# Kernel tuning notes

Hardware: AMD Instinct MI355X
Metric: run time of the kernel (lower is better)

The kernel has to match this reference:

```python
import jax, jax.numpy as jnp
import numpy as np

B, C, D, H, W, N = 1, 48, 64, 64, 64, 16


def setup_inputs() -> dict:
    key = jax.random.key(0)
    ks = jax.random.split(key, 7)
    x = jax.random.normal(ks[0], (B, C, D, H, W), jnp.float32)
    # Per-direction S6 parameters (3 scan directions: D, H, W axes)
    A_log = jax.random.normal(ks[1], (3, C, N), jnp.float32) * 0.5
    W_dt = jax.random.normal(ks[2], (3, C, C), jnp.float32) * (0.5 / np.sqrt(C))
    b_dt = jax.random.normal(ks[3], (3, C), jnp.float32) * 0.1
    W_B = jax.random.normal(ks[4], (3, C, N), jnp.float32) / np.sqrt(C)
    W_C = jax.random.normal(ks[5], (3, C, N), jnp.float32) / np.sqrt(C)
    D_skip = jnp.ones((3, C), jnp.float32)
    return dict(x=x, A_log=A_log, W_dt=W_dt, b_dt=b_dt, W_B=W_B, W_C=W_C, D_skip=D_skip)


def _dir_scan(xl, dt, Bc, Cc, A, Dskip, axis):
    """Selective scan along one spatial axis.
    xl, dt: [B,D,H,W,C]; Bc, Cc: [B,D,H,W,N]; A: [C,N]; Dskip: [C]."""
    L = xl.shape[axis]

    def to_seq(t):
        t = jnp.moveaxis(t, axis, 0)          # [L, ..., F]
        return t.reshape(L, -1, t.shape[-1])  # [L, M, F]

    xs, dts, Bs, Cs = to_seq(xl), to_seq(dt), to_seq(Bc), to_seq(Cc)
    M = xs.shape[1]

    def step(h, inp):
        x_t, dt_t, B_t, C_t = inp              # [M,C],[M,C],[M,N],[M,N]
        decay = jnp.exp(dt_t[:, :, None] * A)  # [M,C,N]
        h = decay * h + (dt_t * x_t)[:, :, None] * B_t[:, None, :]
        y = jnp.einsum('mcn,mn->mc', h, C_t) + Dskip * x_t
        return h, y

    h0 = jnp.zeros((M, xs.shape[2], A.shape[-1]), xl.dtype)
    _, ys = jax.lax.scan(step, h0, (xs, dts, Bs, Cs))  # ys: [L, M, C]
    seq_shape = jnp.moveaxis(xl, axis, 0).shape
    return jnp.moveaxis(ys.reshape(seq_shape), 0, axis)


def reference(x, A_log, W_dt, b_dt, W_B, W_C, D_skip):
    xl = jnp.moveaxis(x, 1, -1)  # [B,D,H,W,C]
    y = jnp.zeros_like(xl)
    for d, axis in enumerate((1, 2, 3)):  # scan along D, H, W
        A = -jnp.exp(A_log[d])                       # [C,N], negative -> stable
        dt = jax.nn.softplus(xl @ W_dt[d] + b_dt[d])  # [B,D,H,W,C]
        Bc = xl @ W_B[d]                              # [B,D,H,W,N]
        Cc = xl @ W_C[d]                              # [B,D,H,W,N]
        y = y + _dir_scan(xl, dt, Bc, Cc, A, D_skip[d], axis)
    return jnp.moveaxis(y, -1, 1)  # [B,C,D,H,W]
```

## Files before the change

kernel.cpp:

```cpp
#include <hip/hip_runtime.h>
#include <math.h>

#define CCH 48
#define NST 16
#define VOX (64*64*64)

__device__ __forceinline__ float softplus_f(float s) {
    return fmaxf(s, 0.f) + log1pf(__expf(-fabsf(s)));
}

template<int CTRL>
__device__ __forceinline__ float dpp_add(float x) {
    int v = __builtin_amdgcn_update_dpp(0, __float_as_int(x), CTRL, 0xF, 0xF, true);
    return x + __int_as_float(v);
}

__global__ __launch_bounds__(256) void k_transpose_in(const float* __restrict__ x,
                                                      float* __restrict__ xt) {
    __shared__ float tile[CCH * 65];
    int v0 = blockIdx.x * 64;
    int t = threadIdx.x;
#pragma unroll
    for (int i = 0; i < 12; ++i) {
        int idx = t + i * 256;
        int c = idx >> 6, v = idx & 63;
        tile[c * 65 + v] = x[c * VOX + v0 + v];
    }
    __syncthreads();
#pragma unroll
    for (int i = 0; i < 12; ++i) {
        int idx = t + i * 256;
        int v = idx / CCH, c = idx - v * CCH;
        xt[(v0 + v) * CCH + c] = tile[c * 65 + v];
    }
}

__global__ __launch_bounds__(256) void k_transpose_out(const float* __restrict__ yws,
                                                       float* __restrict__ out) {
    __shared__ float tile[CCH * 65];
    int v0 = blockIdx.x * 64;
    int t = threadIdx.x;
#pragma unroll
    for (int i = 0; i < 12; ++i) {
        int idx = t + i * 256;
        int v = idx / CCH, c = idx - v * CCH;
        tile[c * 65 + v] = yws[(v0 + v) * CCH + c];
    }
    __syncthreads();
#pragma unroll
    for (int i = 0; i < 12; ++i) {
        int idx = t + i * 256;
        int c = idx >> 6, v = idx & 63;
        out[c * VOX + v0 + v] = tile[c * 65 + v];
    }
}

#define OFF_XS    0
#define OFF_WDT   3072
#define OFF_WB    5568
#define OFF_WC    6400
#define OFF_DTS   7232
#define OFF_UX    10496
#define OFF_BC    13760
#define OFF_CC    14848
#define OFF_YS    3072
#define SMEM_FLOATS 15936

__global__ __launch_bounds__(768, 6) void k_scan(
    const float* __restrict__ xt, float* __restrict__ yws,
    const float* __restrict__ A_log, const float* __restrict__ W_dt,
    const float* __restrict__ b_dt, const float* __restrict__ W_B,
    const float* __restrict__ W_C, const float* __restrict__ D_skip,
    int dir, int stride_v, int accumulate)
{
    __shared__ __align__(16) float smem[SMEM_FLOATS];
    float* xs   = smem + OFF_XS;
    float* wdtT = smem + OFF_WDT;
    float* wBT  = smem + OFF_WB;
    float* wCT  = smem + OFF_WC;
    float* dtsT = smem + OFF_DTS;
    float* uxT  = smem + OFF_UX;
    float* BcsT = smem + OFF_BC;
    float* CcsT = smem + OFF_CC;
    float* ys   = smem + OFF_YS;

    int t = threadIdx.x;
    int lid = blockIdx.x;
    int a = lid >> 6, b = lid & 63;
    int vbase;
    if (dir == 0) vbase = lid;
    else if (dir == 1) vbase = a * 4096 + b;
    else vbase = a * 4096 + b * 64;

    const float* wdt_g = W_dt + dir * CCH * CCH;
    const float* wB_g  = W_B + dir * CCH * NST;
    const float* wC_g  = W_C + dir * CCH * NST;

    {
        int q = t % 12, l = t / 12;
        *(float4*)&xs[l * CCH + 4 * q] =
            *(const float4*)&xt[(vbase + l * stride_v) * CCH + 4 * q];
    }
    for (int idx = t; idx < CCH * CCH; idx += 768) {
        int k = idx / CCH, c2 = idx - k * CCH;
        wdtT[c2 * 52 + k] = wdt_g[idx];
    }
    {
        int k = t >> 4, n2 = t & 15;
        wBT[n2 * 52 + k] = wB_g[t];
        wCT[n2 * 52 + k] = wC_g[t];
    }
    __syncthreads();

    {
        int c  = t % CCH;
        int l0 = t / CCH;
        float bc = b_dt[dir * CCH + c];
        const float4* wr  = (const float4*)&wdtT[c * 52];
        const float4* xr0 = (const float4*)&xs[(4 * l0 + 0) * CCH];
        const float4* xr1 = (const float4*)&xs[(4 * l0 + 1) * CCH];
        const float4* xr2 = (const float4*)&xs[(4 * l0 + 2) * CCH];
        const float4* xr3 = (const float4*)&xs[(4 * l0 + 3) * CCH];
        float s0 = bc, s1 = bc, s2 = bc, s3 = bc;
#pragma unroll
        for (int q = 0; q < 12; ++q) {
            float4 wv = wr[q];
            float4 x0 = xr0[q], x1 = xr1[q], x2 = xr2[q], x3 = xr3[q];
            s0 = fmaf(x0.x, wv.x, s0); s0 = fmaf(x0.y, wv.y, s0);
            s0 = fmaf(x0.z, wv.z, s0); s0 = fmaf(x0.w, wv.w, s0);
            s1 = fmaf(x1.x, wv.x, s1); s1 = fmaf(x1.y, wv.y, s1);
            s1 = fmaf(x1.z, wv.z, s1); s1 = fmaf(x1.w, wv.w, s1);
            s2 = fmaf(x2.x, wv.x, s2); s2 = fmaf(x2.y, wv.y, s2);
            s2 = fmaf(x2.z, wv.z, s2); s2 = fmaf(x2.w, wv.w, s2);
            s3 = fmaf(x3.x, wv.x, s3); s3 = fmaf(x3.y, wv.y, s3);
            s3 = fmaf(x3.z, wv.z, s3); s3 = fmaf(x3.w, wv.w, s3);
        }
        float4 dtv, uxv;
        dtv.x = softplus_f(s0); uxv.x = dtv.x * xs[(4 * l0 + 0) * CCH + c];
        dtv.y = softplus_f(s1); uxv.y = dtv.y * xs[(4 * l0 + 1) * CCH + c];
        dtv.z = softplus_f(s2); uxv.z = dtv.z * xs[(4 * l0 + 2) * CCH + c];
        dtv.w = softplus_f(s3); uxv.w = dtv.w * xs[(4 * l0 + 3) * CCH + c];
        *(float4*)&dtsT[c * 68 + 4 * l0] = dtv;
        *(float4*)&uxT[c * 68 + 4 * l0]  = uxv;
    }
    {
        int n = t & 15;
        int lA = t >> 4;
#pragma unroll
        for (int rep = 0; rep < 2; ++rep) {
            int l = (rep == 0) ? lA : (48 + lA);
            if (rep == 0 || t < 256) {
                const float4* xr  = (const float4*)&xs[l * CCH];
                const float4* wbr = (const float4*)&wBT[n * 52];
                const float4* wcr = (const float4*)&wCT[n * 52];
                float sB = 0.f, sC = 0.f;
#pragma unroll
                for (int q = 0; q < 12; ++q) {
                    float4 xv = xr[q];
                    float4 wb = wbr[q];
                    float4 wc = wcr[q];
                    sB = fmaf(xv.x, wb.x, sB); sC = fmaf(xv.x, wc.x, sC);
                    sB = fmaf(xv.y, wb.y, sB); sC = fmaf(xv.y, wc.y, sC);
                    sB = fmaf(xv.z, wb.z, sB); sC = fmaf(xv.z, wc.z, sC);
                    sB = fmaf(xv.w, wb.w, sB); sC = fmaf(xv.w, wc.w, sC);
                }
                BcsT[n * 68 + l] = sB;
                CcsT[n * 68 + l] = sC;
            }
        }
    }
    __syncthreads();

    if (t < 384) {
        int cc = t >> 3, nh = t & 7;
        float a0 = -expf(A_log[dir * CCH * NST + cc * NST + nh]);
        float a1 = -expf(A_log[dir * CCH * NST + cc * NST + nh + 8]);
        const float4* dt4 = (const float4*)&dtsT[cc * 68];
        const float4* ux4 = (const float4*)&uxT[cc * 68];
        const float4* B4a = (const float4*)&BcsT[nh * 68];
        const float4* B4b = (const float4*)&BcsT[(nh + 8) * 68];
        const float4* C4a = (const float4*)&CcsT[nh * 68];
        const float4* C4b = (const float4*)&CcsT[(nh + 8) * 68];
        float h0 = 0.f, h1 = 0.f;

#define STEP(COMP, LIDX)                                                    \
        {                                                                   \
            float e0 = __expf(dtv.COMP * a0);                               \
            float e1 = __expf(dtv.COMP * a1);                               \
            h0 = fmaf(e0, h0, uxv.COMP * Bva.COMP);                         \
            h1 = fmaf(e1, h1, uxv.COMP * Bvb.COMP);                         \
            float p = fmaf(h1, Cvb.COMP, h0 * Cva.COMP);                    \
            p = dpp_add<0xB1>(p);                                           \
            p = dpp_add<0x4E>(p);                                           \
            p = dpp_add<0x141>(p);                                          \
            if (nh == 0) ys[(LIDX) * CCH + cc] = p;                         \
        }

#pragma unroll
        for (int l4 = 0; l4 < 16; ++l4) {
            float4 dtv = dt4[l4];
            float4 uxv = ux4[l4];
            float4 Bva = B4a[l4];
            float4 Bvb = B4b[l4];
            float4 Cva = C4a[l4];
            float4 Cvb = C4b[l4];
            STEP(x, l4 * 4 + 0)
            STEP(y, l4 * 4 + 1)
            STEP(z, l4 * 4 + 2)
            STEP(w, l4 * 4 + 3)
        }
#undef STEP
    }
    __syncthreads();

    {
        int q = t % 12, l = t / 12;
        float4 yv = *(const float4*)&ys[l * CCH + 4 * q];
        float4 xv = *(const float4*)&xs[l * CCH + 4 * q];
        float4 dv = *(const float4*)&D_skip[dir * CCH + 4 * q];
        yv.x = fmaf(dv.x, xv.x, yv.x);
        yv.y = fmaf(dv.y, xv.y, yv.y);
        yv.z = fmaf(dv.z, xv.z, yv.z);
        yv.w = fmaf(dv.w, xv.w, yv.w);
        float* gp = &yws[(vbase + l * stride_v) * CCH + 4 * q];
        if (accumulate) {
            float4 old = *(const float4*)gp;
            yv.x += old.x; yv.y += old.y; yv.z += old.z; yv.w += old.w;
        }
        *(float4*)gp = yv;
    }
}

extern "C" void kernel_launch(void* const* d_in, const int* in_sizes, int n_in,
                              void* d_out, int out_size, void* d_ws, size_t ws_size,
                              hipStream_t stream) {
    const float* x      = (const float*)d_in[0];
    const float* A_log  = (const float*)d_in[1];
    const float* W_dt   = (const float*)d_in[2];
    const float* b_dt   = (const float*)d_in[3];
    const float* W_B    = (const float*)d_in[4];
    const float* W_C    = (const float*)d_in[5];
    const float* D_skip = (const float*)d_in[6];
    float* out = (float*)d_out;

    float* xt  = (float*)d_ws;
    float* yws = xt + (size_t)VOX * CCH;

    k_transpose_in<<<VOX / 64, 256, 0, stream>>>(x, xt);
    k_scan<<<4096, 768, 0, stream>>>(xt, yws, A_log, W_dt, b_dt, W_B, W_C, D_skip, 0, 4096, 0);
    k_scan<<<4096, 768, 0, stream>>>(xt, yws, A_log, W_dt, b_dt, W_B, W_C, D_skip, 1, 64, 1);
    k_scan<<<4096, 768, 0, stream>>>(xt, yws, A_log, W_dt, b_dt, W_B, W_C, D_skip, 2, 1, 1);
    k_transpose_out<<<VOX / 64, 256, 0, stream>>>(yws, out);
}
```

Baseline: 390.2 us.

## Compute dt/B/C projections with bf16 MFMA instead of scalar FMA

Replaces the per-thread fp32 FMA projections of x onto W_dt, W_B and W_C with one fused 80x48 by 48x64 matrix product on bf16 MFMA (16x16x32) instructions, using bf16 copies of x and the weights staged in shared memory with K padded to 64. This is meant to cut the VALU and LDS-read cost of the projection phase before the scan. In exchange it adds conversion work, an extra sync and some extra shared memory, and bf16 rounding of the projection inputs lowers precision, which could hurt accuracy.

Measured after the change: 360.8 us. 7.5% less time.

```diff
diff --git a/kernel.cpp b/kernel.cpp
--- a/kernel.cpp
+++ b/kernel.cpp
@@ -5,8 +5,18 @@
 #define NST 16
 #define VOX (64*64*64)
 
+typedef __attribute__((ext_vector_type(8))) short bf16x8_t;
+typedef __attribute__((ext_vector_type(4))) float f32x4_t;
+typedef unsigned short ushort_t;
+
 __device__ __forceinline__ float softplus_f(float s) {
     return fmaxf(s, 0.f) + log1pf(__expf(-fabsf(s)));
+}
+
+__device__ __forceinline__ ushort_t f2bf(float f) {
+    unsigned u = __float_as_uint(f);
+    unsigned r = (u + 0x7FFF + ((u >> 16) & 1)) >> 16;
+    return (ushort_t)r;
 }
 
 template<int CTRL>
@@ -56,15 +66,14 @@
 }
 
 #define OFF_XS    0
-#define OFF_WDT   3072
-#define OFF_WB    5568
-#define OFF_WC    6400
-#define OFF_DTS   7232
-#define OFF_UX    10496
-#define OFF_BC    13760
-#define OFF_CC    14848
+#define OFF_XB    3072
+#define OFF_WB16  5376
+#define OFF_DTS   8256
+#define OFF_UX    11520
+#define OFF_BC    14784
+#define OFF_CC    15872
 #define OFF_YS    3072
-#define SMEM_FLOATS 15936
+#define SMEM_FLOATS 16960
 
 __global__ __launch_bounds__(768, 6) void k_scan(
     const float* __restrict__ xt, float* __restrict__ yws,
@@ -75,14 +84,13 @@
 {
     __shared__ __align__(16) float smem[SMEM_FLOATS];
     float* xs   = smem + OFF_XS;
-    float* wdtT = smem + OFF_WDT;
-    float* wBT  = smem + OFF_WB;
-    float* wCT  = smem + OFF_WC;
     float* dtsT = smem + OFF_DTS;
     float* uxT  = smem + OFF_UX;
     float* BcsT = smem + OFF_BC;
     float* CcsT = smem + OFF_CC;
     float* ys   = smem + OFF_YS;
+    ushort_t* xb = (ushort_t*)(smem + OFF_XB);
+    ushort_t* wb = (ushort_t*)(smem + OFF_WB16);
 
     int t = threadIdx.x;
     int lid = blockIdx.x;
@@ -98,76 +106,66 @@
 
     {
         int q = t % 12, l = t / 12;
-        *(float4*)&xs[l * CCH + 4 * q] =
-            *(const float4*)&xt[(vbase + l * stride_v) * CCH + 4 * q];
-    }
-    for (int idx = t; idx < CCH * CCH; idx += 768) {
-        int k = idx / CCH, c2 = idx - k * CCH;
-        wdtT[c2 * 52 + k] = wdt_g[idx];
-    }
-    {
-        int k = t >> 4, n2 = t & 15;
-        wBT[n2 * 52 + k] = wB_g[t];
-        wCT[n2 * 52 + k] = wC_g[t];
-    }
-    __syncthreads();
-
-    {
-        int c  = t % CCH;
-        int l0 = t / CCH;
-        float bc = b_dt[dir * CCH + c];
-        const float4* wr  = (const float4*)&wdtT[c * 52];
-        const float4* xr0 = (const float4*)&xs[(4 * l0 + 0) * CCH];
-        const float4* xr1 = (const float4*)&xs[(4 * l0 + 1) * CCH];
-        const float4* xr2 = (const float4*)&xs[(4 * l0 + 2) * CCH];
-        const float4* xr3 = (const float4*)&xs[(4 * l0 + 3) * CCH];
-        float s0 = bc, s1 = bc, s2 = bc, s3 = bc;
-#pragma unroll
-        for (int q = 0; q < 12; ++q) {
-            float4 wv = wr[q];
-            float4 x0 = xr0[q], x1 = xr1[q], x2 = xr2[q], x3 = xr3[q];
-            s0 = fmaf(x0.x, wv.x, s0); s0 = fmaf(x0.y, wv.y, s0);
-            s0 = fmaf(x0.z, wv.z, s0); s0 = fmaf(x0.w, wv.w, s0);
-            s1 = fmaf(x1.x, wv.x, s1); s1 = fmaf(x1.y, wv.y, s1);
-            s1 = fmaf(x1.z, wv.z, s1); s1 = fmaf(x1.w, wv.w, s1);
-            s2 = fmaf(x2.x, wv.x, s2); s2 = fmaf(x2.y, wv.y, s2);
-            s2 = fmaf(x2.z, wv.z, s2); s2 = fmaf(x2.w, wv.w, s2);
-            s3 = fmaf(x3.x, wv.x, s3); s3 = fmaf(x3.y, wv.y, s3);
-            s3 = fmaf(x3.z, wv.z, s3); s3 = fmaf(x3.w, wv.w, s3);
-        }
+        float4 v = *(const float4*)&xt[(vbase + l * stride_v) * CCH + 4 * q];
+        *(float4*)&xs[l * CCH + 4 * q] = v;
+        unsigned p0 = (unsigned)f2bf(v.x) | ((unsigned)f2bf(v.y) << 16);
+        unsigned p1 = (unsigned)f2bf(v.z) | ((unsigned)f2bf(v.w) << 16);
+        unsigned* d = (unsigned*)&xb[l * 72 + 4 * q];
+        d[0] = p0; d[1] = p1;
+    }
+    for (int idx = t; idx < 3840; idx += 768) {
+        float v; int row, k;
+        if (idx < 2304)      { k = idx / 48;       row = idx % 48;        v = wdt_g[idx]; }
+        else if (idx < 3072) { int j = idx - 2304; k = j >> 4; row = 48 + (j & 15); v = wB_g[j]; }
+        else                 { int j = idx - 3072; k = j >> 4; row = 64 + (j & 15); v = wC_g[j]; }
+        wb[row * 72 + k] = f2bf(v);
+    }
+    for (int i = t; i < 80 * 16; i += 768) wb[(i >> 4) * 72 + 48 + (i & 15)] = 0;
+    for (int i = t; i < 64 * 16; i += 768) xb[(i >> 4) * 72 + 48 + (i & 15)] = 0;
+    __syncthreads();
+
+    {
+        int w = t >> 6, lane = t & 63;
+        if (w < 10) {
+            int r16 = lane & 15, g = lane >> 4;
+#pragma unroll
+            for (int tt = 0; tt < 2; ++tt) {
+                int tile = w * 2 + tt;
+                int tm = tile >> 2, tn = tile & 3;
+                const ushort_t* ap = &wb[(tm * 16 + r16) * 72 + g * 8];
+                const ushort_t* bp = &xb[(tn * 16 + r16) * 72 + g * 8];
+                bf16x8_t A0 = *(const bf16x8_t*)ap;
+                bf16x8_t A1 = *(const bf16x8_t*)(ap + 32);
+                bf16x8_t B0 = *(const bf16x8_t*)bp;
+                bf16x8_t B1 = *(const bf16x8_t*)(bp + 32);
+                f32x4_t acc = {0.f, 0.f, 0.f, 0.f};
+                acc = __builtin_amdgcn_mfma_f32_16x16x32_bf16(A0, B0, acc, 0, 0, 0);
+                acc = __builtin_amdgcn_mfma_f32_16x16x32_bf16(A1, B1, acc, 0, 0, 0);
+                int col = tn * 16 + r16;
+                float* outp;
+                if (tm < 3)       outp = &dtsT[(tm * 16 + g * 4) * 68 + col];
+                else if (tm == 3) outp = &BcsT[(g * 4) * 68 + col];
+                else              outp = &CcsT[(g * 4) * 68 + col];
+                outp[0 * 68] = acc[0];
+                outp[1 * 68] = acc[1];
+                outp[2 * 68] = acc[2];
+                outp[3 * 68] = acc[3];
+            }
+        }
+    }
+    __syncthreads();
+
+    {
+        int c = t % CCH, l0 = t / CCH;
+        float bias = b_dt[dir * CCH + c];
+        float4 dv = *(const float4*)&dtsT[c * 68 + 4 * l0];
         float4 dtv, uxv;
-        dtv.x = softplus_f(s0); uxv.x = dtv.x * xs[(4 * l0 + 0) * CCH + c];
-        dtv.y = softplus_f(s1); uxv.y = dtv.y * xs[(4 * l0 + 1) * CCH + c];
-        dtv.z = softplus_f(s2); uxv.z = dtv.z * xs[(4 * l0 + 2) * CCH + c];
-        dtv.w = softplus_f(s3); uxv.w = dtv.w * xs[(4 * l0 + 3) * CCH + c];
+        dtv.x = softplus_f(dv.x + bias); uxv.x = dtv.x * xs[(4 * l0 + 0) * CCH + c];
+        dtv.y = softplus_f(dv.y + bias); uxv.y = dtv.y * xs[(4 * l0 + 1) * CCH + c];
+        dtv.z = softplus_f(dv.z + bias); uxv.z = dtv.z * xs[(4 * l0 + 2) * CCH + c];
+        dtv.w = softplus_f(dv.w + bias); uxv.w = dtv.w * xs[(4 * l0 + 3) * CCH + c];
         *(float4*)&dtsT[c * 68 + 4 * l0] = dtv;
         *(float4*)&uxT[c * 68 + 4 * l0]  = uxv;
-    }
-    {
-        int n = t & 15;
-        int lA = t >> 4;
-#pragma unroll
-        for (int rep = 0; rep < 2; ++rep) {
-            int l = (rep == 0) ? lA : (48 + lA);
-            if (rep == 0 || t < 256) {
-                const float4* xr  = (const float4*)&xs[l * CCH];
-                const float4* wbr = (const float4*)&wBT[n * 52];
-                const float4* wcr = (const float4*)&wCT[n * 52];
-                float sB = 0.f, sC = 0.f;
-#pragma unroll
-                for (int q = 0; q < 12; ++q) {
-                    float4 xv = xr[q];
-                    float4 wb = wbr[q];
-                    float4 wc = wcr[q];
-                    sB = fmaf(xv.x, wb.x, sB); sC = fmaf(xv.x, wc.x, sC);
-                    sB = fmaf(xv.y, wb.y, sB); sC = fmaf(xv.y, wc.y, sC);
-                    sB = fmaf(xv.z, wb.z, sB); sC = fmaf(xv.z, wc.z, sC);
-                    sB = fmaf(xv.w, wb.w, sB); sC = fmaf(xv.w, wc.w, sC);
-                }
-                BcsT[n * 68 + l] = sB;
-                CcsT[n * 68 + l] = sC;
-            }
-        }
     }
     __syncthreads();
 
```
